# Kernel optimization log

Hardware: AMD Instinct MI355X
Metric: run time of the kernel (lower is better)

## Reference

```python
import jax, jax.numpy as jnp
import numpy as np

B, S, H = 4, 2048, 1024

def setup_inputs() -> dict:
    key = jax.random.key(0)
    ks = jax.random.split(key, 6)
    scale = 1.0 / np.sqrt(H)
    return {
        "query": jax.random.normal(ks[0], (B, S, H), dtype=jnp.float32),
        "key":   jax.random.normal(ks[1], (B, S, H), dtype=jnp.float32),
        "value": jax.random.normal(ks[2], (B, S, H), dtype=jnp.float32),
        "Wq": jax.random.normal(ks[3], (H, H), dtype=jnp.float32) * scale,
        "Wk": jax.random.normal(ks[4], (H, H), dtype=jnp.float32) * scale,
        "Wv": jax.random.normal(ks[5], (H, H), dtype=jnp.float32) * scale,
    }

def reference(query, key, value, Wq, Wk, Wv):
    # nn.Linear(bias=False): y = x @ W.T
    q = jnp.einsum('bsh,oh->bso', query, Wq)
    k = jnp.einsum('bsh,oh->bso', key, Wk)
    v = jnp.einsum('bsh,oh->bso', value, Wv)
    # full QK^T scores [B, Q, K], scaled by sqrt(hidden_size)
    scores = jnp.einsum('bqh,bkh->bqk', q, k) / jnp.sqrt(jnp.asarray(H, q.dtype))
    attn = jax.nn.softmax(scores, axis=2)
    return jnp.einsum('bqk,bkh->bqh', attn, v)
```

## Files before the change

kernel.cpp:

```cpp
#include <hip/hip_runtime.h>
#include <hip/hip_bf16.h>
#include <stdint.h>

#define BATCH 4
#define SLEN  2048
#define HID   1024

typedef __attribute__((ext_vector_type(8))) short bfrag8;
typedef __attribute__((ext_vector_type(4))) float facc4;
typedef __attribute__((ext_vector_type(4))) unsigned short us4;

__device__ __forceinline__ unsigned short f2b(float f) {
  union { float f; unsigned int i; } x; x.f = f;
  unsigned int r = x.i + 0x7FFFu + ((x.i >> 16) & 1u);
  return (unsigned short)(r >> 16);
}

__device__ __forceinline__ void gl_lds16(const void* g, void* l) {
  __builtin_amdgcn_global_load_lds(
      (const __attribute__((address_space(1))) void*)g,
      (__attribute__((address_space(3))) void*)l, 16, 0, 0);
}

__global__ __launch_bounds__(256) void cast_all(
    const float* __restrict__ q, const float* __restrict__ k,
    const float* __restrict__ v, const float* __restrict__ wq,
    const float* __restrict__ wk, const float* __restrict__ wv,
    us4* __restrict__ dst, float* __restrict__ lsum) {
  if (blockIdx.x < 8) {
    float4 z = {0.f, 0.f, 0.f, 0.f};
    ((float4*)lsum)[blockIdx.x * 256 + threadIdx.x] = z;
  }
  const long i = (long)blockIdx.x * 256 + threadIdx.x;
  const long S1 = 2097152, S2 = 4194304, S3 = 6291456,
             S4 = 6553600, S5 = 6815744;
  const float4* src; long off;
  if (i < S2) {
    if (i < S1) { src = (const float4*)q;  off = i; }
    else        { src = (const float4*)k;  off = i - S1; }
  } else if (i < S3) { src = (const float4*)v;  off = i - S2; }
  else if   (i < S4) { src = (const float4*)wq; off = i - S3; }
  else if   (i < S5) { src = (const float4*)wk; off = i - S4; }
  else               { src = (const float4*)wv; off = i - S5; }
  float4 x = src[off];
  us4 o;
  o.x = f2b(x.x); o.y = f2b(x.y); o.z = f2b(x.z); o.w = f2b(x.w);
  dst[i] = o;
}

__device__ __forceinline__ void core256(
    const unsigned short* __restrict__ A, const unsigned short* __restrict__ B,
    const int lda, const int ldb, const int NT,
    unsigned short* __restrict__ As, unsigned short* __restrict__ Bs,
    facc4 (&acc)[8][4]) {
  const int tid  = threadIdx.x;
  const int lane = tid & 63;
  const int wave = tid >> 6;
  const int wm = wave >> 2;
  const int wn = wave & 3;
  const int ln = lane & 15;
  const int lq = lane >> 4;
  const int swz = ln & 7;

  const int row0 = tid >> 3;
  const int blk  = (tid & 7) ^ (row0 & 7);
  const unsigned short* pA = A + (long)row0 * lda + blk * 8;
  const unsigned short* pB = B + (long)row0 * ldb + blk * 8;
  const long a64 = 64l * lda, b64 = 64l * ldb;
  unsigned short* dA = As + tid * 8;
  unsigned short* dB = Bs + tid * 8;

#define STG_A(h, b, t) do { const unsigned short* g_ = pA + (h) * (a64 * 2) + (long)(t) * 64; \
    gl_lds16(g_,       dA + (b) * 16384 + (h) * 8192); \
    gl_lds16(g_ + a64, dA + (b) * 16384 + (h) * 8192 + 4096); } while (0)
#define STG_B(h, b, t) do { const unsigned short* g_ = pB + (h) * (b64 * 2) + (long)(t) * 64; \
    gl_lds16(g_,       dB + (b) * 16384 + (h) * 8192); \
    gl_lds16(g_ + b64, dB + (b) * 16384 + (h) * 8192 + 4096); } while (0)

  const int o0 = (lq ^ swz) * 8;
  const int o1 = ((4 + lq) ^ swz) * 8;
  const int aOfs = wm * 8192 + ln * 64;
  const int bOfs = (wn >> 1) * 8192 + ((wn & 1) * 64 + ln) * 64;

  STG_A(0, 0, 0); STG_A(1, 0, 0); STG_B(0, 0, 0); STG_B(1, 0, 0);
  STG_A(0, 1, 1); STG_A(1, 1, 1);
  asm volatile("s_waitcnt vmcnt(4)" ::: "memory");
  __builtin_amdgcn_s_barrier();

#define MFMA16(AF, BF, MOFS, NOFS)                                          \
  _Pragma("unroll") for (int m_ = 0; m_ < 4; ++m_)                          \
  _Pragma("unroll") for (int n_ = 0; n_ < 2; ++n_) {                        \
    acc[(MOFS) + m_][(NOFS) + n_] = __builtin_amdgcn_mfma_f32_16x16x32_bf16(\
        AF[m_][0], BF[n_][0], acc[(MOFS) + m_][(NOFS) + n_], 0, 0, 0);      \
    acc[(MOFS) + m_][(NOFS) + n_] = __builtin_amdgcn_mfma_f32_16x16x32_bf16(\
        AF[m_][1], BF[n_][1], acc[(MOFS) + m_][(NOFS) + n_], 0, 0, 0);      \
  }

  for (int t = 0; t < NT; ++t) {
    const int bu = t & 1, nx = bu ^ 1;
    const unsigned short* Ab = As + bu * 16384 + aOfs;
    const unsigned short* Bb = Bs + bu * 16384 + bOfs;
    bfrag8 a0[4][2], a1[4][2], b0[2][2], b1[2][2];

#pragma unroll
    for (int m = 0; m < 4; ++m) {
      a0[m][0] = *(const bfrag8*)(Ab + m * 1024 + o0);
      a0[m][1] = *(const bfrag8*)(Ab + m * 1024 + o1);
    }
#pragma unroll
    for (int n = 0; n < 2; ++n) {
      b0[n][0] = *(const bfrag8*)(Bb + n * 1024 + o0);
      b0[n][1] = *(const bfrag8*)(Bb + n * 1024 + o1);
    }
    if (t + 1 < NT) STG_B(0, nx, t + 1);
    __builtin_amdgcn_s_barrier();
    __builtin_amdgcn_s_setprio(1);
    MFMA16(a0, b0, 0, 0)
    __builtin_amdgcn_s_setprio(0);
    __builtin_amdgcn_s_barrier();

#pragma unroll
    for (int m = 0; m < 4; ++m) {
      a1[m][0] = *(const bfrag8*)(Ab + (4 + m) * 1024 + o0);
      a1[m][1] = *(const bfrag8*)(Ab + (4 + m) * 1024 + o1);
    }
#pragma unroll
    for (int n = 0; n < 2; ++n) {
      b1[n][0] = *(const bfrag8*)(Bb + (2 + n) * 1024 + o0);
      b1[n][1] = *(const bfrag8*)(Bb + (2 + n) * 1024 + o1);
    }
    if (t + 1 < NT) STG_B(1, nx, t + 1);
    __builtin_amdgcn_s_barrier();
    __builtin_amdgcn_s_setprio(1);
    MFMA16(a1, b1, 4, 2)
    __builtin_amdgcn_s_setprio(0);
    __builtin_amdgcn_s_barrier();

    if (t + 2 < NT) STG_A(0, bu, t + 2);
    __builtin_amdgcn_s_setprio(1);
    MFMA16(a0, b1, 0, 2)
    __builtin_amdgcn_s_setprio(0);
    __builtin_amdgcn_s_barrier();

    if (t + 2 < NT) STG_A(1, bu, t + 2);
    __builtin_amdgcn_s_setprio(1);
    MFMA16(a1, b0, 4, 0)
    __builtin_amdgcn_s_setprio(0);
    if (t + 2 < NT) asm volatile("s_waitcnt vmcnt(4)" ::: "memory");
    else            asm volatile("s_waitcnt vmcnt(0)" ::: "memory");
    __builtin_amdgcn_s_barrier();
  }
#undef MFMA16
#undef STG_A
#undef STG_B
}

__global__ __launch_bounds__(512, 2) void proj3_256(
    const unsigned short* __restrict__ Xq, const unsigned short* __restrict__ Wqb,
    const unsigned short* __restrict__ Xk, const unsigned short* __restrict__ Wkb,
    const unsigned short* __restrict__ Xv, const unsigned short* __restrict__ Wvb,
    unsigned short* __restrict__ Qb, unsigned short* __restrict__ Kb,
    unsigned short* __restrict__ Vt) {
  extern __shared__ unsigned short smem[];
  unsigned short* As = smem;
  unsigned short* Bs = smem + 32768;

  const int pid = blockIdx.x;
  const int p2  = (pid & 7) * 48 + (pid >> 3);
  const int g   = p2 >> 7;
  const int within = p2 & 127;

  const unsigned short* A; const unsigned short* B; unsigned short* C;
  long bm, bn; int ldc_;
  if (g == 0)      { A = Xq;  B = Wqb; C = Qb; }
  else if (g == 1) { A = Xk;  B = Wkb; C = Kb; }
  else             { A = Wvb; B = Xv;  C = Vt; }
  if (g < 2) { bm = (long)(within >> 2) * 256; bn = (long)(within & 3)  * 256; ldc_ = 1024; }
  else       { bm = (long)(within >> 5) * 256; bn = (long)(within & 31) * 256; ldc_ = 8192; }

  facc4 acc[8][4] = {};
  core256(A + bm * 1024, B + bn * 1024, 1024, 1024, HID / 64, As, Bs, acc);

  const int lane = threadIdx.x & 63, wave = threadIdx.x >> 6;
  const int wm = wave >> 2, wn = wave & 3;
  const int ln = lane & 15, lq = lane >> 4;
#pragma unroll
  for (int m = 0; m < 8; ++m)
#pragma unroll
    for (int n = 0; n < 4; ++n) {
      const long mm = bm + wm * 128 + m * 16 + lq * 4;
      const long nn = bn + wn * 64 + n * 16 + ln;
#pragma unroll
      for (int r = 0; r < 4; ++r)
        C[(mm + r) * (long)ldc_ + nn] = f2b(acc[m][n][r]);
    }
}

__global__ __launch_bounds__(512, 2) void scores256(
    const unsigned short* __restrict__ Q, const unsigned short* __restrict__ Kb,
    unsigned short* __restrict__ P, float* __restrict__ lsum) {
  extern __shared__ unsigned short smem[];
  unsigned short* As = smem;
  unsigned short* Bs = smem + 32768;

  const long z = blockIdx.z;
  const int pid = blockIdx.y * 8 + blockIdx.x;
  const int p2  = (pid & 7) * 8 + (pid >> 3);
  const long bm = (long)(p2 >> 3) * 256;
  const long bn = (long)(p2 & 7) * 256;

  const long SH = (long)SLEN * HID, SS = (long)SLEN * SLEN;
  facc4 acc[8][4] = {};
  core256(Q + z * SH + bm * 1024, Kb + z * SH + bn * 1024, 1024, 1024,
          HID / 64, As, Bs, acc);

  unsigned short* Pz = P + z * SS;
  float* lz = lsum + z * SLEN;
  const int lane = threadIdx.x & 63, wave = threadIdx.x >> 6;
  const int wm = wave >> 2, wn = wave & 3;
  const int ln = lane & 15, lq = lane >> 4;
#pragma unroll
  for (int m = 0; m < 8; ++m) {
#pragma unroll
    for (int r = 0; r < 4; ++r) {
      const long q = bm + wm * 128 + m * 16 + lq * 4 + r;
      float rowsum = 0.f;
#pragma unroll
      for (int n = 0; n < 4; ++n) {
        const long kcol = bn + wn * 64 + n * 16 + ln;
        float e = __expf(acc[m][n][r] * 0.03125f);
        Pz[q * (long)SLEN + kcol] = f2b(e);
        rowsum += e;
      }
      rowsum += __shfl_xor(rowsum, 1, 64);
      rowsum += __shfl_xor(rowsum, 2, 64);
      rowsum += __shfl_xor(rowsum, 4, 64);
      rowsum += __shfl_xor(rowsum, 8, 64);
      if (ln == 0) atomicAdd(&lz[q], rowsum);
    }
  }
}

template <int MODE, typename OutT>
__global__ __launch_bounds__(256) void gemm_nt(
    const unsigned short* __restrict__ A, const unsigned short* __restrict__ B,
    OutT* __restrict__ C, int K, int lda, int ldb, int ldc,
    long aStrideZ, long bStrideZ, long cStrideZ, float alpha,
    float* __restrict__ lsum) {
  A += (long)blockIdx.z * aStrideZ;
  B += (long)blockIdx.z * bStrideZ;
  C += (long)blockIdx.z * cStrideZ;
  const long lz = (long)blockIdx.z * SLEN;

  const int nbm = gridDim.x, nbn = gridDim.y;
  const int nb  = nbm * nbn;
  const int pid = blockIdx.y * nbm + blockIdx.x;
  const int p2  = (pid & 7) * (nb >> 3) + (pid >> 3);
  const int GROUP = 4;
  const int gsize = GROUP * nbn;
  const int gid   = p2 / gsize;
  const int rem   = p2 - gid * gsize;
  const long bm = (long)(gid * GROUP + (rem & (GROUP - 1))) * 128;
  const long bn = (long)(rem >> 2) * 128;

  __shared__ __align__(16) unsigned short As[128 * 64];
  __shared__ __align__(16) unsigned short Bs[128 * 64];

  const int tid  = threadIdx.x;
  const int lane = tid & 63;
  const int wave = tid >> 6;
  const int wr   = (wave >> 1) * 64;
  const int wc   = (wave & 1) * 64;
  const int ln   = lane & 15;
  const int lq   = lane >> 4;
  const int swz  = ln & 7;

  facc4 acc[4][4] = {};

  const unsigned short* ap[4]; const unsigned short* bp[4];
  unsigned short* asd[4]; unsigned short* bsd[4];
#pragma unroll
  for (int j = 0; j < 4; ++j) {
    const int c   = j * 256 + tid;
    const int row = c >> 3;
    const int src = ((c & 7) ^ (row & 7)) * 8;
    ap[j]  = A + (bm + row) * (long)lda + src;
    bp[j]  = B + (bn + row) * (long)ldb + src;
    asd[j] = &As[c * 8];
    bsd[j] = &Bs[c * 8];
  }

  for (int k0 = 0; k0 < K; k0 += 64) {
#pragma unroll
    for (int j = 0; j < 4; ++j) { gl_lds16(ap[j], asd[j]); ap[j] += 64; }
#pragma unroll
    for (int j = 0; j < 4; ++j) { gl_lds16(bp[j], bsd[j]); bp[j] += 64; }
    __syncthreads();

#pragma unroll
    for (int kk = 0; kk < 2; ++kk) {
      bfrag8 af[4], bfr[4];
#pragma unroll
      for (int i = 0; i < 4; ++i)
        af[i] = *(const bfrag8*)&As[(wr + i * 16 + ln) * 64 + ((kk * 4 + lq) ^ swz) * 8];
#pragma unroll
      for (int j = 0; j < 4; ++j)
        bfr[j] = *(const bfrag8*)&Bs[(wc + j * 16 + ln) * 64 + ((kk * 4 + lq) ^ swz) * 8];
#pragma unroll
      for (int i = 0; i < 4; ++i)
#pragma unroll
        for (int j = 0; j < 4; ++j)
          acc[i][j] = __builtin_amdgcn_mfma_f32_16x16x32_bf16(af[i], bfr[j], acc[i][j], 0, 0, 0);
    }
    __syncthreads();
  }

  if constexpr (MODE == 1) {
#pragma unroll
    for (int i = 0; i < 4; ++i) {
#pragma unroll
      for (int r = 0; r < 4; ++r) {
        const long m = bm + wr + i * 16 + lq * 4 + r;
        float rowsum = 0.f;
#pragma unroll
        for (int j = 0; j < 4; ++j) {
          const long n = bn + wc + j * 16 + ln;
          float e = __expf(acc[i][j][r] * alpha);
          C[m * (long)ldc + n] = (OutT)f2b(e);
          rowsum += e;
        }
        rowsum += __shfl_xor(rowsum, 1, 64);
        rowsum += __shfl_xor(rowsum, 2, 64);
        rowsum += __shfl_xor(rowsum, 4, 64);
        rowsum += __shfl_xor(rowsum, 8, 64);
        if (ln == 0) atomicAdd(&lsum[lz + m], rowsum);
      }
    }
  } else {
    float inv[16];
#pragma unroll
    for (int i = 0; i < 4; ++i)
#pragma unroll
      for (int r = 0; r < 4; ++r)
        inv[i * 4 + r] = 1.0f / lsum[lz + bm + wr + i * 16 + lq * 4 + r];
#pragma unroll
    for (int i = 0; i < 4; ++i)
#pragma unroll
      for (int j = 0; j < 4; ++j) {
        const long m = bm + wr + i * 16 + lq * 4;
        const long n = bn + wc + j * 16 + ln;
#pragma unroll
        for (int r = 0; r < 4; ++r)
          ((float*)C)[(m + r) * (long)ldc + n] = acc[i][j][r] * inv[i * 4 + r];
      }
  }
}

extern "C" void kernel_launch(void* const* d_in, const int* in_sizes, int n_in,
                              void* d_out, int out_size, void* d_ws, size_t ws_size,
                              hipStream_t stream) {
  const float* q_in = (const float*)d_in[0];
  const float* k_in = (const float*)d_in[1];
  const float* v_in = (const float*)d_in[2];
  const float* wq   = (const float*)d_in[3];
  const float* wk   = (const float*)d_in[4];
  const float* wv   = (const float*)d_in[5];
  float* out = (float*)d_out;

  const long NXH = (long)BATCH * SLEN * HID;
  const long NW  = (long)HID * HID;
  const long SH  = (long)SLEN * HID;
  const long SS  = (long)SLEN * SLEN;

  unsigned short* ws = (unsigned short*)d_ws;
  unsigned short* Xq  = ws;
  unsigned short* Xk  = Xq  + NXH;
  unsigned short* Xv  = Xk  + NXH;
  unsigned short* Wqb = Xv  + NXH;
  unsigned short* Wkb = Wqb + NW;
  unsigned short* Wvb = Wkb + NW;
  unsigned short* Qb  = Wvb + NW;
  unsigned short* Kb  = Qb  + NXH;
  unsigned short* Vt  = Kb  + NXH;
  float*          lsum = (float*)(Vt + NXH);
  unsigned short* P   = Xq;

  static bool attr_done = false;
  if (!attr_done) {
    hipFuncSetAttribute(reinterpret_cast<const void*>(proj3_256),
                        hipFuncAttributeMaxDynamicSharedMemorySize, 131072);
    hipFuncSetAttribute(reinterpret_cast<const void*>(scores256),
                        hipFuncAttributeMaxDynamicSharedMemorySize, 131072);
    attr_done = true;
  }

  cast_all<<<dim3(27648), dim3(256), 0, stream>>>(q_in, k_in, v_in, wq, wk, wv,
                                                  (us4*)ws, lsum);

  proj3_256<<<dim3(384), dim3(512), 131072, stream>>>(
      Xq, Wqb, Xk, Wkb, Xv, Wvb, Qb, Kb, Vt);

  scores256<<<dim3(8, 8, BATCH), dim3(512), 131072, stream>>>(Qb, Kb, P, lsum);

  gemm_nt<2, float><<<dim3(16, 8, BATCH), dim3(256), 0, stream>>>(
      P, Vt, out, SLEN, SLEN, BATCH * SLEN, HID, SS, SLEN, SH, 1.0f, lsum);
}
```

Baseline: 294.0 us.

## Restructure GEMM core loop to prefetch next-tile fragments and stage both operands two ahead

Rewrites the shared 256x256 GEMM main loop so that A and B tiles for step t+2 are issued with the LDS-direct loads, and the register fragments for the next step are read from LDS while the current MFMAs run. Barriers drop from five to three per iteration. NT becomes a template parameter so the loop can be fully unrolled. This aims to hide LDS read latency and global load waits behind the matrix instructions, at the cost of extra fragment registers, which could cause spills or lower occupancy under launch_bounds(512,2).

```diff
diff --git a/kernel.cpp b/kernel.cpp
--- a/kernel.cpp
+++ b/kernel.cpp
@@ -48,9 +48,10 @@
   dst[i] = o;
 }
 
+template <int NT>
 __device__ __forceinline__ void core256(
     const unsigned short* __restrict__ A, const unsigned short* __restrict__ B,
-    const int lda, const int ldb, const int NT,
+    const int lda, const int ldb,
     unsigned short* __restrict__ As, unsigned short* __restrict__ Bs,
     facc4 (&acc)[8][4]) {
   const int tid  = threadIdx.x;
@@ -82,75 +83,78 @@
   const int aOfs = wm * 8192 + ln * 64;
   const int bOfs = (wn >> 1) * 8192 + ((wn & 1) * 64 + ln) * 64;
 
-  STG_A(0, 0, 0); STG_A(1, 0, 0); STG_B(0, 0, 0); STG_B(1, 0, 0);
-  STG_A(0, 1, 1); STG_A(1, 1, 1);
-  asm volatile("s_waitcnt vmcnt(4)" ::: "memory");
+#define RD_A4(dst, bufb, mb) do { \
+  _Pragma("unroll") for (int m_ = 0; m_ < 4; ++m_) { \
+    dst[m_][0] = *(const bfrag8*)(As + (bufb) + aOfs + ((mb) + m_) * 1024 + o0); \
+    dst[m_][1] = *(const bfrag8*)(As + (bufb) + aOfs + ((mb) + m_) * 1024 + o1); \
+  } } while (0)
+#define RD_B2(dst, bufb, nb) do { \
+  _Pragma("unroll") for (int n_ = 0; n_ < 2; ++n_) { \
+    dst[n_][0] = *(const bfrag8*)(Bs + (bufb) + bOfs + ((nb) + n_) * 1024 + o0); \
+    dst[n_][1] = *(const bfrag8*)(Bs + (bufb) + bOfs + ((nb) + n_) * 1024 + o1); \
+  } } while (0)
+
+#define MFMAQ(AF, BF, MO, NO) do { \
+  _Pragma("unroll") for (int m_ = 0; m_ < 4; ++m_) \
+  _Pragma("unroll") for (int n_ = 0; n_ < 2; ++n_) { \
+    acc[(MO)+m_][(NO)+n_] = __builtin_amdgcn_mfma_f32_16x16x32_bf16( \
+        AF[m_][0], BF[n_][0], acc[(MO)+m_][(NO)+n_], 0, 0, 0); \
+    acc[(MO)+m_][(NO)+n_] = __builtin_amdgcn_mfma_f32_16x16x32_bf16( \
+        AF[m_][1], BF[n_][1], acc[(MO)+m_][(NO)+n_], 0, 0, 0); \
+  } } while (0)
+
+  bfrag8 a0[4][2], a1[4][2], b0[2][2], b1[2][2], a0n[4][2], b0n[2][2];
+
+  STG_B(0, 0, 0); STG_A(0, 0, 0); STG_A(1, 0, 0); STG_B(1, 0, 0);
+  STG_B(0, 1, 1); STG_A(0, 1, 1); STG_A(1, 1, 1); STG_B(1, 1, 1);
+  asm volatile("s_waitcnt vmcnt(8)" ::: "memory");
   __builtin_amdgcn_s_barrier();
-
-#define MFMA16(AF, BF, MOFS, NOFS)                                          \
-  _Pragma("unroll") for (int m_ = 0; m_ < 4; ++m_)                          \
-  _Pragma("unroll") for (int n_ = 0; n_ < 2; ++n_) {                        \
-    acc[(MOFS) + m_][(NOFS) + n_] = __builtin_amdgcn_mfma_f32_16x16x32_bf16(\
-        AF[m_][0], BF[n_][0], acc[(MOFS) + m_][(NOFS) + n_], 0, 0, 0);      \
-    acc[(MOFS) + m_][(NOFS) + n_] = __builtin_amdgcn_mfma_f32_16x16x32_bf16(\
-        AF[m_][1], BF[n_][1], acc[(MOFS) + m_][(NOFS) + n_], 0, 0, 0);      \
-  }
-
+  RD_A4(a0, 0, 0);
+  RD_B2(b0, 0, 0);
+
+#pragma unroll
   for (int t = 0; t < NT; ++t) {
-    const int bu = t & 1, nx = bu ^ 1;
-    const unsigned short* Ab = As + bu * 16384 + aOfs;
-    const unsigned short* Bb = Bs + bu * 16384 + bOfs;
-    bfrag8 a0[4][2], a1[4][2], b0[2][2], b1[2][2];
-
-#pragma unroll
-    for (int m = 0; m < 4; ++m) {
-      a0[m][0] = *(const bfrag8*)(Ab + m * 1024 + o0);
-      a0[m][1] = *(const bfrag8*)(Ab + m * 1024 + o1);
-    }
-#pragma unroll
-    for (int n = 0; n < 2; ++n) {
-      b0[n][0] = *(const bfrag8*)(Bb + n * 1024 + o0);
-      b0[n][1] = *(const bfrag8*)(Bb + n * 1024 + o1);
-    }
-    if (t + 1 < NT) STG_B(0, nx, t + 1);
-    __builtin_amdgcn_s_barrier();
+    const int bb = (t & 1) * 16384;
+    const int nb = bb ^ 16384;
+
+    RD_B2(b1, bb, 2);
     __builtin_amdgcn_s_setprio(1);
-    MFMA16(a0, b0, 0, 0)
+    MFMAQ(a0, b0, 0, 0);
     __builtin_amdgcn_s_setprio(0);
     __builtin_amdgcn_s_barrier();
 
-#pragma unroll
-    for (int m = 0; m < 4; ++m) {
-      a1[m][0] = *(const bfrag8*)(Ab + (4 + m) * 1024 + o0);
-      a1[m][1] = *(const bfrag8*)(Ab + (4 + m) * 1024 + o1);
-    }
-#pragma unroll
-    for (int n = 0; n < 2; ++n) {
-      b1[n][0] = *(const bfrag8*)(Bb + (2 + n) * 1024 + o0);
-      b1[n][1] = *(const bfrag8*)(Bb + (2 + n) * 1024 + o1);
-    }
-    if (t + 1 < NT) STG_B(1, nx, t + 1);
+    RD_A4(a1, bb, 4);
+    if (t + 2 < NT) STG_B(0, t & 1, t + 2);
+    __builtin_amdgcn_s_setprio(1);
+    MFMAQ(a0, b1, 0, 2);
+    __builtin_amdgcn_s_setprio(0);
+    if (t + 2 < NT) asm volatile("s_waitcnt vmcnt(2)" ::: "memory");
+    else            asm volatile("s_waitcnt vmcnt(0)" ::: "memory");
     __builtin_amdgcn_s_barrier();
+
+    if (t + 1 < NT) RD_A4(a0n, nb, 0);
+    if (t + 2 < NT) STG_A(0, t & 1, t + 2);
     __builtin_amdgcn_s_setprio(1);
-    MFMA16(a1, b1, 4, 2)
+    MFMAQ(a1, b1, 4, 2);
+    __builtin_amdgcn_s_setprio(0);
+
+    if (t + 1 < NT) RD_B2(b0n, nb, 0);
+    if (t + 2 < NT) { STG_A(1, t & 1, t + 2); STG_B(1, t & 1, t + 2); }
+    __builtin_amdgcn_s_setprio(1);
+    MFMAQ(a1, b0, 4, 0);
     __builtin_amdgcn_s_setprio(0);
     __builtin_amdgcn_s_barrier();
 
-    if (t + 2 < NT) STG_A(0, bu, t + 2);
-    __builtin_amdgcn_s_setprio(1);
-    MFMA16(a0, b1, 0, 2)
-    __builtin_amdgcn_s_setprio(0);
-    __builtin_amdgcn_s_barrier();
-
-    if (t + 2 < NT) STG_A(1, bu, t + 2);
-    __builtin_amdgcn_s_setprio(1);
-    MFMA16(a1, b0, 4, 0)
-    __builtin_amdgcn_s_setprio(0);
-    if (t + 2 < NT) asm volatile("s_waitcnt vmcnt(4)" ::: "memory");
-    else            asm volatile("s_waitcnt vmcnt(0)" ::: "memory");
-    __builtin_amdgcn_s_barrier();
-  }
-#undef MFMA16
+    if (t + 1 < NT) {
+#pragma unroll
+      for (int m_ = 0; m_ < 4; ++m_) { a0[m_][0] = a0n[m_][0]; a0[m_][1] = a0n[m_][1]; }
+#pragma unroll
+      for (int n_ = 0; n_ < 2; ++n_) { b0[n_][0] = b0n[n_][0]; b0[n_][1] = b0n[n_][1]; }
+    }
+  }
+#undef MFMAQ
+#undef RD_A4
+#undef RD_B2
 #undef STG_A
 #undef STG_B
 }
@@ -179,7 +183,7 @@
   else       { bm = (long)(within >> 5) * 256; bn = (long)(within & 31) * 256; ldc_ = 8192; }
 
   facc4 acc[8][4] = {};
-  core256(A + bm * 1024, B + bn * 1024, 1024, 1024, HID / 64, As, Bs, acc);
+  core256<HID / 64>(A + bm * 1024, B + bn * 1024, 1024, 1024, As, Bs, acc);
 
   const int lane = threadIdx.x & 63, wave = threadIdx.x >> 6;
   const int wm = wave >> 2, wn = wave & 3;
@@ -211,8 +215,8 @@
 
   const long SH = (long)SLEN * HID, SS = (long)SLEN * SLEN;
   facc4 acc[8][4] = {};
-  core256(Q + z * SH + bm * 1024, Kb + z * SH + bn * 1024, 1024, 1024,
-          HID / 64, As, Bs, acc);
+  core256<HID / 64>(Q + z * SH + bm * 1024, Kb + z * SH + bn * 1024, 1024, 1024,
+                    As, Bs, acc);
 
   unsigned short* Pz = P + z * SS;
   float* lz = lsum + z * SLEN;
```

Measured after the change: 288.2 us. 1.02x faster.
